# Optimization experiments

Measured on AMD Instinct MI355X. Metric: run time of the kernel, lower is better.

## Reference

```python
import jax, jax.numpy as jnp
import numpy as np


def setup_inputs() -> dict:
    key = jax.random.key(0)
    k1, k2, k3, k4 = jax.random.split(key, 4)
    B, T, C, H = 8, 2048, 1024, 1024
    return {
        "x": jax.random.normal(k1, (B, T, C), dtype=jnp.float32),
        "Wk": jax.random.normal(k2, (H, C), dtype=jnp.float32),
        "Wq": jax.random.normal(k3, (H, C), dtype=jnp.float32),
        "Wv": jax.random.normal(k4, (H, C), dtype=jnp.float32),
    }


def reference(x, Wk, Wq, Wv):
    # x: [B, T, C]; Wk/Wq/Wv: [H, C] (torch Linear stores [fan_out, fan_in])
    B, T, C = x.shape
    k = jnp.einsum('btc,hc->bth', x, Wk)  # [B, T, H]
    q = jnp.einsum('btc,hc->bth', x, Wq)
    v = jnp.einsum('btc,hc->bth', x, Wv)
    # NOTE: source scales by n_embd (C) ** -0.5, not head_size
    wei = jnp.einsum('bth,bsh->bts', q, k) * (C ** -0.5)  # [B, T, T]
    causal = jnp.tril(jnp.ones((T, T), dtype=bool))
    wei = jnp.where(causal, wei, -jnp.inf)
    wei = jax.nn.softmax(wei, axis=-1)
    # Dropout omitted (inference behavior; p=0.5 train-only in source)
    out = jnp.einsum('bts,bsh->bth', wei, v)  # [B, T, H]
    return (out, wei)
```

## Files before the change

### kernel.cpp

```cpp
#include <hip/hip_runtime.h>
#include <hip/hip_bf16.h>


#define BB 8
#define TT 2048
#define CC 1024
#define HH 1024
#define BT (BB * TT)

typedef _Float16 f16x8 __attribute__((ext_vector_type(8)));
typedef _Float16 f16x4 __attribute__((ext_vector_type(4)));
typedef float f32x4 __attribute__((ext_vector_type(4)));

#define AS1 __attribute__((address_space(1)))
#define AS3 __attribute__((address_space(3)))

__device__ __forceinline__ void gld16(const _Float16* g, _Float16* lds) {
    __builtin_amdgcn_global_load_lds((AS1 const unsigned int*)g,
                                     (AS3 unsigned int*)lds, 16, 0, 0);
}

__global__ __launch_bounds__(256) void split_kernel(
    const float* __restrict__ src, _Float16* __restrict__ dh,
    _Float16* __restrict__ dl, int n)
{
    int i = (blockIdx.x * 256 + threadIdx.x) * 4;
    if (i >= n) return;
    float4 v = *(const float4*)(src + i);
    f16x4 h, l;
    h[0] = (_Float16)v.x; l[0] = (_Float16)(v.x - (float)h[0]);
    h[1] = (_Float16)v.y; l[1] = (_Float16)(v.y - (float)h[1]);
    h[2] = (_Float16)v.z; l[2] = (_Float16)(v.z - (float)h[2]);
    h[3] = (_Float16)v.w; l[3] = (_Float16)(v.w - (float)h[3]);
    *(f16x4*)&dh[i] = h;
    *(f16x4*)&dl[i] = l;
}

__global__ __launch_bounds__(256) void splitT_kernel(
    const float* __restrict__ W, _Float16* __restrict__ th,
    _Float16* __restrict__ tl)
{
    __shared__ float L[64][65];
    const int h0 = blockIdx.x * 64;
    const int c0 = blockIdx.y * 64;
    const int tid = threadIdx.x;
    {
        const int hl = tid >> 2;
        const int cs = (tid & 3) * 16;
#pragma unroll
        for (int jj = 0; jj < 16; jj += 4) {
            float4 v = *(const float4*)&W[(size_t)(h0 + hl) * CC + c0 + cs + jj];
            L[cs + jj + 0][hl] = v.x;
            L[cs + jj + 1][hl] = v.y;
            L[cs + jj + 2][hl] = v.z;
            L[cs + jj + 3][hl] = v.w;
        }
    }
    __syncthreads();
    const int c  = tid >> 2;
    const int hs = (tid & 3) * 16;
    f16x8 hv0, hv1, lv0, lv1;
#pragma unroll
    for (int i = 0; i < 8; ++i) {
        float a = L[c][hs + i], b = L[c][hs + 8 + i];
        hv0[i] = (_Float16)a; lv0[i] = (_Float16)(a - (float)hv0[i]);
        hv1[i] = (_Float16)b; lv1[i] = (_Float16)(b - (float)hv1[i]);
    }
    size_t o = (size_t)(c0 + c) * HH + h0 + hs;
    *(f16x8*)&th[o] = hv0; *(f16x8*)&th[o + 8] = hv1;
    *(f16x8*)&tl[o] = lv0; *(f16x8*)&tl[o + 8] = lv1;
}

__global__ __launch_bounds__(256, 2) void mm_kernel(
    const _Float16* __restrict__ aH, const _Float16* __restrict__ aL,
    const _Float16* __restrict__ bH, const _Float16* __restrict__ bL,
    _Float16* __restrict__ mtH, _Float16* __restrict__ mtL)
{
    __shared__ _Float16 Ah[4096], Al[4096], Bh[4096], Bl[4096];

    const int n0 = blockIdx.x * 128;
    const int m0 = blockIdx.y * 128;

    const int tid  = threadIdx.x;
    const int r0   = tid & 127;
    const int k0   = tid >> 7;
    const int wave = tid >> 6;
    const int lane = tid & 63;
    const int quad = lane >> 4;
    const int lrow = lane & 15;
    const int wr   = (wave >> 1) * 64;
    const int wc   = (wave & 1) * 64;

    const size_t ga = (size_t)(m0 + r0) * HH + k0 * 8;
    const size_t gb = (size_t)(n0 + r0) * HH + k0 * 8;
    const int lds0 = tid * 8, lds1 = (tid + 256) * 8;

    f32x4 acc[4][4] = {};

    for (int kc = 0; kc < HH; kc += 32) {
        __syncthreads();
        gld16(aH + ga + kc,      &Ah[lds0]);
        gld16(aH + ga + kc + 16, &Ah[lds1]);
        gld16(aL + ga + kc,      &Al[lds0]);
        gld16(aL + ga + kc + 16, &Al[lds1]);
        gld16(bH + gb + kc,      &Bh[lds0]);
        gld16(bH + gb + kc + 16, &Bh[lds1]);
        gld16(bL + gb + kc,      &Bl[lds0]);
        gld16(bL + gb + kc + 16, &Bl[lds1]);
        __syncthreads();

        f16x8 ahf[4], alf[4], bhf[4], blf[4];
#pragma unroll
        for (int i = 0; i < 4; ++i) {
            ahf[i] = *(const f16x8*)&Ah[(quad * 128 + wr + i * 16 + lrow) * 8];
            alf[i] = *(const f16x8*)&Al[(quad * 128 + wr + i * 16 + lrow) * 8];
            bhf[i] = *(const f16x8*)&Bh[(quad * 128 + wc + i * 16 + lrow) * 8];
            blf[i] = *(const f16x8*)&Bl[(quad * 128 + wc + i * 16 + lrow) * 8];
        }
#pragma unroll
        for (int i = 0; i < 4; ++i)
#pragma unroll
            for (int j = 0; j < 4; ++j) {
                acc[i][j] = __builtin_amdgcn_mfma_f32_16x16x32_f16(ahf[i], bhf[j], acc[i][j], 0, 0, 0);
                acc[i][j] = __builtin_amdgcn_mfma_f32_16x16x32_f16(ahf[i], blf[j], acc[i][j], 0, 0, 0);
                acc[i][j] = __builtin_amdgcn_mfma_f32_16x16x32_f16(alf[i], bhf[j], acc[i][j], 0, 0, 0);
            }
    }

#pragma unroll
    for (int i = 0; i < 4; ++i)
#pragma unroll
        for (int j = 0; j < 4; ++j) {
            int mm = m0 + wr + i * 16 + quad * 4;
            int nn = n0 + wc + j * 16 + lrow;
            f16x4 ph, pl;
#pragma unroll
            for (int r = 0; r < 4; ++r) {
                float val = acc[i][j][r];
                _Float16 h = (_Float16)val;
                ph[r] = h;
                pl[r] = (_Float16)(val - (float)h);
            }
            *(f16x4*)&mtH[(size_t)nn * CC + mm] = ph;
            *(f16x4*)&mtL[(size_t)nn * CC + mm] = pl;
        }
}

#define EPI_STRIDE 136
__global__ __launch_bounds__(256, 2) void pv_kernel(
    const _Float16* __restrict__ xh, const _Float16* __restrict__ xl,
    const _Float16* __restrict__ mtH, const _Float16* __restrict__ mtL,
    const _Float16* __restrict__ Wvh,
    _Float16* __restrict__ Ph, _Float16* __restrict__ Pl,
    _Float16* __restrict__ vT)
{
    __shared__ _Float16 S[32768];

    const int idx   = blockIdx.x;
    const int z     = idx >> 10;
    const int r     = idx & 1023;
    const int xcd   = r & 7;
    const int j7    = r >> 3;
    const int mtile = xcd * 16 + (j7 >> 3);
    const int ntile = j7 & 7;
    const int m0 = mtile * 128;
    const int n0 = ntile * 128;

    const _Float16* Bsrc = (z == 0) ? mtH : Wvh;

    const int tid  = threadIdx.x;
    const int r0   = tid & 127;
    const int k0   = tid >> 7;
    const int wave = tid >> 6;
    const int lane = tid & 63;
    const int quad = lane >> 4;
    const int lrow = lane & 15;
    const int wr   = (wave >> 1) * 64;
    const int wc   = (wave & 1) * 64;

    const size_t ga = (size_t)(m0 + r0) * CC + k0 * 8;
    const size_t gb = (size_t)(n0 + r0) * CC + k0 * 8;
    const int lds0 = tid * 8, lds1 = (tid + 256) * 8;

    f32x4 acc[4][4] = {};

    gld16(xh   + ga,      &S[lds0]);
    gld16(xh   + ga + 16, &S[lds1]);
    gld16(Bsrc + gb,      &S[8192 + lds0]);
    gld16(Bsrc + gb + 16, &S[8192 + lds1]);
    if (z == 0) {
        gld16(xl  + ga,      &S[4096 + lds0]);
        gld16(xl  + ga + 16, &S[4096 + lds1]);
        gld16(mtL + gb,      &S[12288 + lds0]);
        gld16(mtL + gb + 16, &S[12288 + lds1]);
    }
    __syncthreads();

    int cur = 0;
    for (int kc = 0; kc < CC; kc += 32) {
        const int bo = cur << 14;
        const int bn = bo ^ 16384;

        if (kc + 32 < CC) {
            gld16(xh   + ga + kc + 32, &S[bn + lds0]);
            gld16(xh   + ga + kc + 48, &S[bn + lds1]);
            gld16(Bsrc + gb + kc + 32, &S[bn + 8192 + lds0]);
            gld16(Bsrc + gb + kc + 48, &S[bn + 8192 + lds1]);
            if (z == 0) {
                gld16(xl  + ga + kc + 32, &S[bn + 4096 + lds0]);
                gld16(xl  + ga + kc + 48, &S[bn + 4096 + lds1]);
                gld16(mtL + gb + kc + 32, &S[bn + 12288 + lds0]);
                gld16(mtL + gb + kc + 48, &S[bn + 12288 + lds1]);
            }
        }

        const _Float16* Ah = S + bo;
        const _Float16* Al = Ah + 4096;
        const _Float16* Bh = Ah + 8192;
        const _Float16* Bl = Ah + 12288;

        f16x8 ahf[4], bhf[4];
#pragma unroll
        for (int i = 0; i < 4; ++i) {
            ahf[i] = *(const f16x8*)&Ah[(quad * 128 + wr + i * 16 + lrow) * 8];
            bhf[i] = *(const f16x8*)&Bh[(quad * 128 + wc + i * 16 + lrow) * 8];
        }
        if (z == 0) {
            f16x8 alf[4], blf[4];
#pragma unroll
            for (int i = 0; i < 4; ++i) {
                alf[i] = *(const f16x8*)&Al[(quad * 128 + wr + i * 16 + lrow) * 8];
                blf[i] = *(const f16x8*)&Bl[(quad * 128 + wc + i * 16 + lrow) * 8];
            }
#pragma unroll
            for (int i = 0; i < 4; ++i)
#pragma unroll
                for (int j = 0; j < 4; ++j) {
                    acc[i][j] = __builtin_amdgcn_mfma_f32_16x16x32_f16(ahf[i], bhf[j], acc[i][j], 0, 0, 0);
                    acc[i][j] = __builtin_amdgcn_mfma_f32_16x16x32_f16(ahf[i], blf[j], acc[i][j], 0, 0, 0);
                    acc[i][j] = __builtin_amdgcn_mfma_f32_16x16x32_f16(alf[i], bhf[j], acc[i][j], 0, 0, 0);
                }
        } else {
#pragma unroll
            for (int i = 0; i < 4; ++i)
#pragma unroll
                for (int j = 0; j < 4; ++j)
                    acc[i][j] = __builtin_amdgcn_mfma_f32_16x16x32_f16(ahf[i], bhf[j], acc[i][j], 0, 0, 0);
        }

        __syncthreads();
        cur ^= 1;
    }

    if (z == 1) {
#pragma unroll
        for (int i = 0; i < 4; ++i)
#pragma unroll
            for (int j = 0; j < 4; ++j) {
                int hl = wc + j * 16 + lrow;
                int tl = wr + i * 16 + quad * 4;
                f16x4 p;
#pragma unroll
                for (int rr = 0; rr < 4; ++rr) p[rr] = (_Float16)acc[i][j][rr];
                *(f16x4*)&S[hl * EPI_STRIDE + tl] = p;
            }
        __syncthreads();
        const int bi  = mtile >> 4;
        const int t0g = (mtile & 15) * 128;
        _Float16* vb = vT + (size_t)bi * HH * TT;
#pragma unroll
        for (int rr = 0; rr < 128; rr += 16) {
            int h = rr + (tid >> 4);
            int t = (tid & 15) * 8;
            f16x8 val = *(const f16x8*)&S[h * EPI_STRIDE + t];
            *(f16x8*)&vb[(size_t)(n0 + h) * TT + t0g + t] = val;
        }
    } else {
#pragma unroll
        for (int i = 0; i < 4; ++i)
#pragma unroll
            for (int j = 0; j < 4; ++j) {
                int tl = wr + i * 16 + quad * 4;
                int cl = wc + j * 16 + lrow;
#pragma unroll
                for (int rr = 0; rr < 4; ++rr)
                    S[(tl + rr) * EPI_STRIDE + cl] = (_Float16)acc[i][j][rr];
            }
        __syncthreads();
#pragma unroll
        for (int rr = 0; rr < 128; rr += 16) {
            int t = rr + (tid >> 4);
            int c = (tid & 15) * 8;
            f16x8 val = *(const f16x8*)&S[t * EPI_STRIDE + c];
            *(f16x8*)&Ph[(size_t)(m0 + t) * CC + n0 + c] = val;
        }
        __syncthreads();
#pragma unroll
        for (int i = 0; i < 4; ++i)
#pragma unroll
            for (int j = 0; j < 4; ++j) {
                int tl = wr + i * 16 + quad * 4;
                int cl = wc + j * 16 + lrow;
#pragma unroll
                for (int rr = 0; rr < 4; ++rr) {
                    float val = acc[i][j][rr];
                    _Float16 h = (_Float16)val;
                    S[(tl + rr) * EPI_STRIDE + cl] = (_Float16)(val - (float)h);
                }
            }
        __syncthreads();
#pragma unroll
        for (int rr = 0; rr < 128; rr += 16) {
            int t = rr + (tid >> 4);
            int c = (tid & 15) * 8;
            f16x8 val = *(const f16x8*)&S[t * EPI_STRIDE + c];
            *(f16x8*)&Pl[(size_t)(m0 + t) * CC + n0 + c] = val;
        }
    }
}

__global__ __launch_bounds__(256, 2) void logits_kernel(
    const _Float16* __restrict__ Ph, const _Float16* __restrict__ Pl,
    const _Float16* __restrict__ xh, const _Float16* __restrict__ xl,
    float* __restrict__ wei)
{
    __shared__ _Float16 S[32768];

    const int id  = blockIdx.x;
    const int b   = id & 7;
    const int tri = id >> 3;
    int tt = (int)((sqrtf(8.0f * (float)tri + 1.0f) - 1.0f) * 0.5f);
    while ((tt + 1) * (tt + 2) / 2 <= tri) ++tt;
    while (tt * (tt + 1) / 2 > tri) --tt;
    const int st = tri - tt * (tt + 1) / 2;

    const size_t base = (size_t)b * TT * CC;
    float* wb = wei + (size_t)b * TT * TT;
    const int m0 = tt * 128;
    const int n0 = st * 128;

    const int tid  = threadIdx.x;
    const int r0   = tid & 127;
    const int k0   = tid >> 7;
    const int wave = tid >> 6;
    const int lane = tid & 63;
    const int quad = lane >> 4;
    const int lrow = lane & 15;
    const int wr   = (wave >> 1) * 64;
    const int wc   = (wave & 1) * 64;

    const size_t ga = base + (size_t)(m0 + r0) * CC + k0 * 8;
    const size_t gb = base + (size_t)(n0 + r0) * CC + k0 * 8;
    const int lds0 = tid * 8, lds1 = (tid + 256) * 8;

    f32x4 acc[4][4] = {};

    gld16(Ph + ga,      &S[lds0]);
    gld16(Ph + ga + 16, &S[lds1]);
    gld16(Pl + ga,      &S[4096 + lds0]);
    gld16(Pl + ga + 16, &S[4096 + lds1]);
    gld16(xh + gb,      &S[8192 + lds0]);
    gld16(xh + gb + 16, &S[8192 + lds1]);
    gld16(xl + gb,      &S[12288 + lds0]);
    gld16(xl + gb + 16, &S[12288 + lds1]);
    __syncthreads();

    int cur = 0;
    for (int kc = 0; kc < CC; kc += 32) {
        const int bo = cur << 14;
        const int bn = bo ^ 16384;

        if (kc + 32 < CC) {
            gld16(Ph + ga + kc + 32, &S[bn + lds0]);
            gld16(Ph + ga + kc + 48, &S[bn + lds1]);
            gld16(Pl + ga + kc + 32, &S[bn + 4096 + lds0]);
            gld16(Pl + ga + kc + 48, &S[bn + 4096 + lds1]);
            gld16(xh + gb + kc + 32, &S[bn + 8192 + lds0]);
            gld16(xh + gb + kc + 48, &S[bn + 8192 + lds1]);
            gld16(xl + gb + kc + 32, &S[bn + 12288 + lds0]);
            gld16(xl + gb + kc + 48, &S[bn + 12288 + lds1]);
        }

        const _Float16* Ah = S + bo;
        const _Float16* Al = Ah + 4096;
        const _Float16* Bh = Ah + 8192;
        const _Float16* Bl = Ah + 12288;

        f16x8 ahf[4], alf[4], bhf[4], blf[4];
#pragma unroll
        for (int i = 0; i < 4; ++i) {
            ahf[i] = *(const f16x8*)&Ah[(quad * 128 + wr + i * 16 + lrow) * 8];
            alf[i] = *(const f16x8*)&Al[(quad * 128 + wr + i * 16 + lrow) * 8];
            bhf[i] = *(const f16x8*)&Bh[(quad * 128 + wc + i * 16 + lrow) * 8];
            blf[i] = *(const f16x8*)&Bl[(quad * 128 + wc + i * 16 + lrow) * 8];
        }
#pragma unroll
        for (int i = 0; i < 4; ++i)
#pragma unroll
            for (int j = 0; j < 4; ++j) {
                acc[i][j] = __builtin_amdgcn_mfma_f32_16x16x32_f16(ahf[i], bhf[j], acc[i][j], 0, 0, 0);
                acc[i][j] = __builtin_amdgcn_mfma_f32_16x16x32_f16(ahf[i], blf[j], acc[i][j], 0, 0, 0);
                acc[i][j] = __builtin_amdgcn_mfma_f32_16x16x32_f16(alf[i], bhf[j], acc[i][j], 0, 0, 0);
            }

        __syncthreads();
        cur ^= 1;
    }

    const float scale = 0.03125f;
#pragma unroll
    for (int i = 0; i < 4; ++i)
#pragma unroll
        for (int j = 0; j < 4; ++j)
#pragma unroll
            for (int r = 0; r < 4; ++r) {
                int rr = wr + i * 16 + quad * 4 + r;
                int cc = wc + j * 16 + lrow;
                wb[(size_t)(m0 + rr) * TT + n0 + cc] = acc[i][j][r] * scale;
            }
}

__global__ __launch_bounds__(256) void softmax_kernel(
    float* __restrict__ wei, _Float16* __restrict__ wei16)
{
    const int t = blockIdx.x;
    const int b = blockIdx.y;
    float* row = wei + (size_t)b * TT * TT + (size_t)t * TT;
    _Float16* row16 = wei16 + (size_t)b * TT * TT + (size_t)t * TT;
    const int n = t + 1;
    const int tid = threadIdx.x;
    const int base = tid * 8;

    float4 v0 = *(const float4*)&row[base];
    float4 v1 = *(const float4*)&row[base + 4];
    float vals[8] = {v0.x, v0.y, v0.z, v0.w, v1.x, v1.y, v1.z, v1.w};

    float mx = -INFINITY;
#pragma unroll
    for (int i = 0; i < 8; ++i) {
        if (base + i >= n) vals[i] = -INFINITY;
        mx = fmaxf(mx, vals[i]);
    }
#pragma unroll
    for (int off = 32; off > 0; off >>= 1)
        mx = fmaxf(mx, __shfl_down(mx, off));

    __shared__ float redm[4];
    __shared__ float reds[4];
    if ((tid & 63) == 0) redm[tid >> 6] = mx;
    __syncthreads();
    const float m = fmaxf(fmaxf(redm[0], redm[1]), fmaxf(redm[2], redm[3]));

    float sum = 0.f;
#pragma unroll
    for (int i = 0; i < 8; ++i) {
        vals[i] = __expf(vals[i] - m);
        sum += vals[i];
    }
#pragma unroll
    for (int off = 32; off > 0; off >>= 1)
        sum += __shfl_down(sum, off);
    if ((tid & 63) == 0) reds[tid >> 6] = sum;
    __syncthreads();
    const float inv = 1.0f / (reds[0] + reds[1] + reds[2] + reds[3]);

    f16x8 h;
#pragma unroll
    for (int i = 0; i < 8; ++i) {
        float w = vals[i] * inv;
        vals[i] = w;
        h[i] = (_Float16)w;
    }
    *(float4*)&row[base]     = make_float4(vals[0], vals[1], vals[2], vals[3]);
    *(float4*)&row[base + 4] = make_float4(vals[4], vals[5], vals[6], vals[7]);
    *(f16x8*)&row16[base]    = h;
}

__global__ __launch_bounds__(256, 3) void out_kernel(
    const _Float16* __restrict__ wei16, const _Float16* __restrict__ vT,
    float* __restrict__ out)
{
    __shared__ _Float16 S[16384];

    const int id = blockIdx.x;
    const int b  = id & 7;
    const int r  = id >> 3;
    const int tt = 15 - (r >> 3);
    const int nb = r & 7;

    const _Float16* wb = wei16 + (size_t)b * TT * TT;
    const _Float16* vb = vT    + (size_t)b * HH * TT;
    float*          ob = out   + (size_t)b * TT * HH;

    const int m0 = tt * 128;
    const int n0 = nb * 128;
    const int kend = (tt + 1) * 128;

    const int tid  = threadIdx.x;
    const int r0   = tid & 127;
    const int k0   = tid >> 7;
    const int wave = tid >> 6;
    const int lane = tid & 63;
    const int quad = lane >> 4;
    const int lrow = lane & 15;
    const int wr   = (wave >> 1) * 64;
    const int wc   = (wave & 1) * 64;

    const size_t ga = (size_t)(m0 + r0) * TT + k0 * 8;
    const size_t gb = (size_t)(n0 + r0) * TT + k0 * 8;
    const int lds0 = tid * 8, lds1 = (tid + 256) * 8;

    f32x4 acc[4][4] = {};

    gld16(wb + ga,      &S[lds0]);
    gld16(wb + ga + 16, &S[lds1]);
    gld16(vb + gb,      &S[4096 + lds0]);
    gld16(vb + gb + 16, &S[4096 + lds1]);
    __syncthreads();

    int cur = 0;
    for (int kc = 0; kc < kend; kc += 32) {
        const int bo = cur << 13;
        const int bn = bo ^ 8192;

        if (kc + 32 < kend) {
            gld16(wb + ga + kc + 32, &S[bn + lds0]);
            gld16(wb + ga + kc + 48, &S[bn + lds1]);
            gld16(vb + gb + kc + 32, &S[bn + 4096 + lds0]);
            gld16(vb + gb + kc + 48, &S[bn + 4096 + lds1]);
        }

        const _Float16* Ah = S + bo;
        const _Float16* Bh = Ah + 4096;

        f16x8 ahf[4], bhf[4];
#pragma unroll
        for (int i = 0; i < 4; ++i) {
            ahf[i] = *(const f16x8*)&Ah[(quad * 128 + wr + i * 16 + lrow) * 8];
            bhf[i] = *(const f16x8*)&Bh[(quad * 128 + wc + i * 16 + lrow) * 8];
        }
#pragma unroll
        for (int i = 0; i < 4; ++i)
#pragma unroll
            for (int j = 0; j < 4; ++j)
                acc[i][j] = __builtin_amdgcn_mfma_f32_16x16x32_f16(ahf[i], bhf[j], acc[i][j], 0, 0, 0);

        __syncthreads();
        cur ^= 1;
    }

#pragma unroll
    for (int i = 0; i < 4; ++i)
#pragma unroll
        for (int j = 0; j < 4; ++j)
#pragma unroll
            for (int r2 = 0; r2 < 4; ++r2) {
                int rr = wr + i * 16 + quad * 4 + r2;
                int cc = wc + j * 16 + lrow;
                ob[(size_t)(m0 + rr) * HH + n0 + cc] = acc[i][j][r2];
            }
}

extern "C" void kernel_launch(void* const* d_in, const int* in_sizes, int n_in,
                              void* d_out, int out_size, void* d_ws, size_t ws_size,
                              hipStream_t stream)
{
    const float* x  = (const float*)d_in[0];
    const float* Wk = (const float*)d_in[1];
    const float* Wq = (const float*)d_in[2];
    const float* Wv = (const float*)d_in[3];

    const size_t NX = (size_t)BT * CC;
    const size_t NW = (size_t)HH * CC;

    float* out = (float*)d_out;
    float* wei = out + (size_t)BT * HH;

    _Float16* WqTh = (_Float16*)out;
    _Float16* WqTl = WqTh + NW;
    _Float16* WkTh = WqTl + NW;
    _Float16* WkTl = WkTh + NW;
    _Float16* Wvh  = WkTl + NW;
    _Float16* Wvl  = Wvh  + NW;
    _Float16* MTh  = Wvl  + NW;
    _Float16* MTl  = MTh  + NW;

    _Float16* xh = (_Float16*)d_ws;
    _Float16* xl = xh + NX;
    _Float16* Ph = xl + NX;
    _Float16* Pl = Ph + NX;
    _Float16* vT = Pl + NX;
    _Float16* wei16 = (_Float16*)d_ws;

    split_kernel<<<dim3(NX / 1024), 256, 0, stream>>>(x, xh, xl, (int)NX);
    splitT_kernel<<<dim3(HH / 64, CC / 64), 256, 0, stream>>>(Wq, WqTh, WqTl);
    splitT_kernel<<<dim3(HH / 64, CC / 64), 256, 0, stream>>>(Wk, WkTh, WkTl);
    split_kernel<<<dim3(NW / 1024), 256, 0, stream>>>(Wv, Wvh, Wvl, (int)NW);

    mm_kernel<<<dim3(CC / 128, CC / 128), 256, 0, stream>>>(
        WqTh, WqTl, WkTh, WkTl, MTh, MTl);
    pv_kernel<<<dim3(2048), 256, 0, stream>>>(
        xh, xl, MTh, MTl, Wvh, Ph, Pl, vT);
    logits_kernel<<<dim3(136 * BB), 256, 0, stream>>>(
        Ph, Pl, xh, xl, wei);
    softmax_kernel<<<dim3(TT, BB), 256, 0, stream>>>(wei, wei16);
    out_kernel<<<dim3(128 * BB), 256, 0, stream>>>(wei16, vT, out);
}
```

Before: 813.6 us.

## Use three-stage LDS pipeline with single barrier and MFMA priority in GEMM kernels

Converts the double-buffered global_load_lds loops in the pv, logits and out kernels into a triple-buffered pipeline that prefetches two K-steps ahead. It uses an explicit vmcnt wait and one barrier per iteration in place of two __syncthreads, and raises wave priority around the MFMA block. The goal is to hide global load latency and cut barrier stalls, at the cost of 1.5x LDS per block, which may lower occupancy under the launch bounds. Softmax also gains a bounds guard for partial rows.

Result: slower. 832.5 us (+2.3%).

```diff
diff --git a/kernel.cpp b/kernel.cpp
--- a/kernel.cpp
+++ b/kernel.cpp
@@ -154,7 +154,7 @@
     _Float16* __restrict__ Ph, _Float16* __restrict__ Pl,
     _Float16* __restrict__ vT)
 {
-    __shared__ _Float16 S[32768];
+    __shared__ _Float16 S[49152];
 
     const int idx   = blockIdx.x;
     const int z     = idx >> 10;
@@ -166,8 +166,6 @@
     const int m0 = mtile * 128;
     const int n0 = ntile * 128;
 
-    const _Float16* Bsrc = (z == 0) ? mtH : Wvh;
-
     const int tid  = threadIdx.x;
     const int r0   = tid & 127;
     const int k0   = tid >> 7;
@@ -184,54 +182,45 @@
 
     f32x4 acc[4][4] = {};
 
-    gld16(xh   + ga,      &S[lds0]);
-    gld16(xh   + ga + 16, &S[lds1]);
-    gld16(Bsrc + gb,      &S[8192 + lds0]);
-    gld16(Bsrc + gb + 16, &S[8192 + lds1]);
     if (z == 0) {
-        gld16(xl  + ga,      &S[4096 + lds0]);
-        gld16(xl  + ga + 16, &S[4096 + lds1]);
-        gld16(mtL + gb,      &S[12288 + lds0]);
-        gld16(mtL + gb + 16, &S[12288 + lds1]);
-    }
-    __syncthreads();
-
-    int cur = 0;
-    for (int kc = 0; kc < CC; kc += 32) {
-        const int bo = cur << 14;
-        const int bn = bo ^ 16384;
-
-        if (kc + 32 < CC) {
-            gld16(xh   + ga + kc + 32, &S[bn + lds0]);
-            gld16(xh   + ga + kc + 48, &S[bn + lds1]);
-            gld16(Bsrc + gb + kc + 32, &S[bn + 8192 + lds0]);
-            gld16(Bsrc + gb + kc + 48, &S[bn + 8192 + lds1]);
-            if (z == 0) {
-                gld16(xl  + ga + kc + 32, &S[bn + 4096 + lds0]);
-                gld16(xl  + ga + kc + 48, &S[bn + 4096 + lds1]);
-                gld16(mtL + gb + kc + 32, &S[bn + 12288 + lds0]);
-                gld16(mtL + gb + kc + 48, &S[bn + 12288 + lds1]);
-            }
-        }
-
-        const _Float16* Ah = S + bo;
-        const _Float16* Al = Ah + 4096;
-        const _Float16* Bh = Ah + 8192;
-        const _Float16* Bl = Ah + 12288;
-
-        f16x8 ahf[4], bhf[4];
-#pragma unroll
-        for (int i = 0; i < 4; ++i) {
-            ahf[i] = *(const f16x8*)&Ah[(quad * 128 + wr + i * 16 + lrow) * 8];
-            bhf[i] = *(const f16x8*)&Bh[(quad * 128 + wc + i * 16 + lrow) * 8];
-        }
-        if (z == 0) {
-            f16x8 alf[4], blf[4];
+#define PV_STAGE0(kc_, sp_) do { \
+        _Float16* Sb = S + (sp_) * 16384; \
+        gld16(xh  + ga + (kc_),      &Sb[lds0]); \
+        gld16(xh  + ga + (kc_) + 16, &Sb[lds1]); \
+        gld16(xl  + ga + (kc_),      &Sb[4096 + lds0]); \
+        gld16(xl  + ga + (kc_) + 16, &Sb[4096 + lds1]); \
+        gld16(mtH + gb + (kc_),      &Sb[8192 + lds0]); \
+        gld16(mtH + gb + (kc_) + 16, &Sb[8192 + lds1]); \
+        gld16(mtL + gb + (kc_),      &Sb[12288 + lds0]); \
+        gld16(mtL + gb + (kc_) + 16, &Sb[12288 + lds1]); \
+    } while (0)
+        PV_STAGE0(0, 0);
+        PV_STAGE0(32, 1);
+        int sl = 0;
+        for (int kc = 0; kc < CC; kc += 32) {
+            asm volatile("s_waitcnt vmcnt(8)" ::: "memory");
+            __builtin_amdgcn_s_barrier();
+            __builtin_amdgcn_sched_barrier(0);
+
+            int kpre = kc + 64;
+            if (kpre > CC - 32) kpre = CC - 32;
+            int s2 = sl + 2; if (s2 >= 3) s2 -= 3;
+            PV_STAGE0(kpre, s2);
+
+            const _Float16* Ah = S + sl * 16384;
+            const _Float16* Al = Ah + 4096;
+            const _Float16* Bh = Ah + 8192;
+            const _Float16* Bl = Ah + 12288;
+
+            f16x8 ahf[4], alf[4], bhf[4], blf[4];
 #pragma unroll
             for (int i = 0; i < 4; ++i) {
+                ahf[i] = *(const f16x8*)&Ah[(quad * 128 + wr + i * 16 + lrow) * 8];
                 alf[i] = *(const f16x8*)&Al[(quad * 128 + wr + i * 16 + lrow) * 8];
+                bhf[i] = *(const f16x8*)&Bh[(quad * 128 + wc + i * 16 + lrow) * 8];
                 blf[i] = *(const f16x8*)&Bl[(quad * 128 + wc + i * 16 + lrow) * 8];
             }
+            __builtin_amdgcn_s_setprio(1);
 #pragma unroll
             for (int i = 0; i < 4; ++i)
 #pragma unroll
@@ -240,17 +229,54 @@
                     acc[i][j] = __builtin_amdgcn_mfma_f32_16x16x32_f16(ahf[i], blf[j], acc[i][j], 0, 0, 0);
                     acc[i][j] = __builtin_amdgcn_mfma_f32_16x16x32_f16(alf[i], bhf[j], acc[i][j], 0, 0, 0);
                 }
-        } else {
+            __builtin_amdgcn_s_setprio(0);
+
+            ++sl; if (sl == 3) sl = 0;
+        }
+    } else {
+#define PV_STAGE1(kc_, sp_) do { \
+        _Float16* Sb = S + (sp_) * 8192; \
+        gld16(xh  + ga + (kc_),      &Sb[lds0]); \
+        gld16(xh  + ga + (kc_) + 16, &Sb[lds1]); \
+        gld16(Wvh + gb + (kc_),      &Sb[4096 + lds0]); \
+        gld16(Wvh + gb + (kc_) + 16, &Sb[4096 + lds1]); \
+    } while (0)
+        PV_STAGE1(0, 0);
+        PV_STAGE1(32, 1);
+        int sl = 0;
+        for (int kc = 0; kc < CC; kc += 32) {
+            asm volatile("s_waitcnt vmcnt(4)" ::: "memory");
+            __builtin_amdgcn_s_barrier();
+            __builtin_amdgcn_sched_barrier(0);
+
+            int kpre = kc + 64;
+            if (kpre > CC - 32) kpre = CC - 32;
+            int s2 = sl + 2; if (s2 >= 3) s2 -= 3;
+            PV_STAGE1(kpre, s2);
+
+            const _Float16* Ah = S + sl * 8192;
+            const _Float16* Bh = Ah + 4096;
+
+            f16x8 ahf[4], bhf[4];
+#pragma unroll
+            for (int i = 0; i < 4; ++i) {
+                ahf[i] = *(const f16x8*)&Ah[(quad * 128 + wr + i * 16 + lrow) * 8];
+                bhf[i] = *(const f16x8*)&Bh[(quad * 128 + wc + i * 16 + lrow) * 8];
+            }
+            __builtin_amdgcn_s_setprio(1);
 #pragma unroll
             for (int i = 0; i < 4; ++i)
 #pragma unroll
                 for (int j = 0; j < 4; ++j)
                     acc[i][j] = __builtin_amdgcn_mfma_f32_16x16x32_f16(ahf[i], bhf[j], acc[i][j], 0, 0, 0);
-        }
-
-        __syncthreads();
-        cur ^= 1;
-    }
+            __builtin_amdgcn_s_setprio(0);
+
+            ++sl; if (sl == 3) sl = 0;
+        }
+    }
+
+    asm volatile("s_waitcnt vmcnt(0)" ::: "memory");
+    __syncthreads();
 
     if (z == 1) {
 #pragma unroll
@@ -324,7 +350,7 @@
     const _Float16* __restrict__ xh, const _Float16* __restrict__ xl,
     float* __restrict__ wei)
 {
-    __shared__ _Float16 S[32768];
+    __shared__ _Float16 S[49152];
 
     const int id  = blockIdx.x;
     const int b   = id & 7;
@@ -355,33 +381,33 @@
 
     f32x4 acc[4][4] = {};
 
-    gld16(Ph + ga,      &S[lds0]);
-    gld16(Ph + ga + 16, &S[lds1]);
-    gld16(Pl + ga,      &S[4096 + lds0]);
-    gld16(Pl + ga + 16, &S[4096 + lds1]);
-    gld16(xh + gb,      &S[8192 + lds0]);
-    gld16(xh + gb + 16, &S[8192 + lds1]);
-    gld16(xl + gb,      &S[12288 + lds0]);
-    gld16(xl + gb + 16, &S[12288 + lds1]);
-    __syncthreads();
-
-    int cur = 0;
+#define LG_STAGE(kc_, sp_) do { \
+    _Float16* Sb = S + (sp_) * 16384; \
+    gld16(Ph + ga + (kc_),      &Sb[lds0]); \
+    gld16(Ph + ga + (kc_) + 16, &Sb[lds1]); \
+    gld16(Pl + ga + (kc_),      &Sb[4096 + lds0]); \
+    gld16(Pl + ga + (kc_) + 16, &Sb[4096 + lds1]); \
+    gld16(xh + gb + (kc_),      &Sb[8192 + lds0]); \
+    gld16(xh + gb + (kc_) + 16, &Sb[8192 + lds1]); \
+    gld16(xl + gb + (kc_),      &Sb[12288 + lds0]); \
+    gld16(xl + gb + (kc_) + 16, &Sb[12288 + lds1]); \
+} while (0)
+
+    LG_STAGE(0, 0);
+    LG_STAGE(32, 1);
+
+    int sl = 0;
     for (int kc = 0; kc < CC; kc += 32) {
-        const int bo = cur << 14;
-        const int bn = bo ^ 16384;
-
-        if (kc + 32 < CC) {
-            gld16(Ph + ga + kc + 32, &S[bn + lds0]);
-            gld16(Ph + ga + kc + 48, &S[bn + lds1]);
-            gld16(Pl + ga + kc + 32, &S[bn + 4096 + lds0]);
-            gld16(Pl + ga + kc + 48, &S[bn + 4096 + lds1]);
-            gld16(xh + gb + kc + 32, &S[bn + 8192 + lds0]);
-            gld16(xh + gb + kc + 48, &S[bn + 8192 + lds1]);
-            gld16(xl + gb + kc + 32, &S[bn + 12288 + lds0]);
-            gld16(xl + gb + kc + 48, &S[bn + 12288 + lds1]);
-        }
-
-        const _Float16* Ah = S + bo;
+        asm volatile("s_waitcnt vmcnt(8)" ::: "memory");
+        __builtin_amdgcn_s_barrier();
+        __builtin_amdgcn_sched_barrier(0);
+
+        int kpre = kc + 64;
+        if (kpre > CC - 32) kpre = CC - 32;
+        int s2 = sl + 2; if (s2 >= 3) s2 -= 3;
+        LG_STAGE(kpre, s2);
+
+        const _Float16* Ah = S + sl * 16384;
         const _Float16* Al = Ah + 4096;
         const _Float16* Bh = Ah + 8192;
         const _Float16* Bl = Ah + 12288;
@@ -394,6 +420,7 @@
             bhf[i] = *(const f16x8*)&Bh[(quad * 128 + wc + i * 16 + lrow) * 8];
             blf[i] = *(const f16x8*)&Bl[(quad * 128 + wc + i * 16 + lrow) * 8];
         }
+        __builtin_amdgcn_s_setprio(1);
 #pragma unroll
         for (int i = 0; i < 4; ++i)
 #pragma unroll
@@ -402,10 +429,12 @@
                 acc[i][j] = __builtin_amdgcn_mfma_f32_16x16x32_f16(ahf[i], blf[j], acc[i][j], 0, 0, 0);
                 acc[i][j] = __builtin_amdgcn_mfma_f32_16x16x32_f16(alf[i], bhf[j], acc[i][j], 0, 0, 0);
             }
-
-        __syncthreads();
-        cur ^= 1;
-    }
+        __builtin_amdgcn_s_setprio(0);
+
+        ++sl; if (sl == 3) sl = 0;
+    }
+
+    asm volatile("s_waitcnt vmcnt(0)" ::: "memory");
 
     const float scale = 0.03125f;
 #pragma unroll
@@ -431,9 +460,16 @@
     const int tid = threadIdx.x;
     const int base = tid * 8;
 
-    float4 v0 = *(const float4*)&row[base];
-    float4 v1 = *(const float4*)&row[base + 4];
-    float vals[8] = {v0.x, v0.y, v0.z, v0.w, v1.x, v1.y, v1.z, v1.w};
+    float vals[8];
+    if (base < n) {
+        float4 v0 = *(const float4*)&row[base];
+        float4 v1 = *(const float4*)&row[base + 4];
+        vals[0] = v0.x; vals[1] = v0.y; vals[2] = v0.z; vals[3] = v0.w;
+        vals[4] = v1.x; vals[5] = v1.y; vals[6] = v1.z; vals[7] = v1.w;
+    } else {
+#pragma unroll
+        for (int i = 0; i < 8; ++i) vals[i] = -INFINITY;
+    }
 
     float mx = -INFINITY;
 #pragma unroll
@@ -480,7 +516,7 @@
     const _Float16* __restrict__ wei16, const _Float16* __restrict__ vT,
     float* __restrict__ out)
 {
-    __shared__ _Float16 S[16384];
+    __shared__ _Float16 S[24576];
 
     const int id = blockIdx.x;
     const int b  = id & 7;
@@ -512,25 +548,29 @@
 
     f32x4 acc[4][4] = {};
 
-    gld16(wb + ga,      &S[lds0]);
-    gld16(wb + ga + 16, &S[lds1]);
-    gld16(vb + gb,      &S[4096 + lds0]);
-    gld16(vb + gb + 16, &S[4096 + lds1]);
-    __syncthreads();
-
-    int cur = 0;
+#define OUT_STAGE(kc_, sp_) do { \
+    _Float16* Sb = S + (sp_) * 8192; \
+    gld16(wb + ga + (kc_),      &Sb[lds0]); \
+    gld16(wb + ga + (kc_) + 16, &Sb[lds1]); \
+    gld16(vb + gb + (kc_),      &Sb[4096 + lds0]); \
+    gld16(vb + gb + (kc_) + 16, &Sb[4096 + lds1]); \
+} while (0)
+
+    OUT_STAGE(0, 0);
+    OUT_STAGE(32, 1);
+
+    int sl = 0;
     for (int kc = 0; kc < kend; kc += 32) {
-        const int bo = cur << 13;
-        const int bn = bo ^ 8192;
-
-        if (kc + 32 < kend) {
-            gld16(wb + ga + kc + 32, &S[bn + lds0]);
-            gld16(wb + ga + kc + 48, &S[bn + lds1]);
-            gld16(vb + gb + kc + 32, &S[bn + 4096 + lds0]);
-            gld16(vb + gb + kc + 48, &S[bn + 4096 + lds1]);
-        }
-
-        const _Float16* Ah = S + bo;
+        asm volatile("s_waitcnt vmcnt(4)" ::: "memory");
+        __builtin_amdgcn_s_barrier();
+        __builtin_amdgcn_sched_barrier(0);
+
+        int kpre = kc + 64;
+        if (kpre > kend - 32) kpre = kend - 32;
+        int s2 = sl + 2; if (s2 >= 3) s2 -= 3;
+        OUT_STAGE(kpre, s2);
+
+        const _Float16* Ah = S + sl * 8192;
         const _Float16* Bh = Ah + 4096;
 
         f16x8 ahf[4], bhf[4];
@@ -539,15 +579,18 @@
             ahf[i] = *(const f16x8*)&Ah[(quad * 128 + wr + i * 16 + lrow) * 8];
             bhf[i] = *(const f16x8*)&Bh[(quad * 128 + wc + i * 16 + lrow) * 8];
         }
+        __builtin_amdgcn_s_setprio(1);
 #pragma unroll
         for (int i = 0; i < 4; ++i)
 #pragma unroll
             for (int j = 0; j < 4; ++j)
                 acc[i][j] = __builtin_amdgcn_mfma_f32_16x16x32_f16(ahf[i], bhf[j], acc[i][j], 0, 0, 0);
-
-        __syncthreads();
-        cur ^= 1;
-    }
+        __builtin_amdgcn_s_setprio(0);
+
+        ++sl; if (sl == 3) sl = 0;
+    }
+
+    asm volatile("s_waitcnt vmcnt(0)" ::: "memory");
 
 #pragma unroll
     for (int i = 0; i < 4; ++i)
```
